# Kernel tuning notes

Measured on AMD Instinct MI355X. Metric: run time of the kernel, lower is better.

Reference implementation:

```python
import jax, jax.numpy as jnp
import numpy as np

# SLAYER SRM-alpha neuron params (nmnist.yaml defaults)
THETA = 10.0      # spike threshold
TAU_SR = 10.0     # PSP (alpha kernel) time constant
TAU_REF = 1.0     # refractory time constant
SCALE_REF = 2.0   # refractory amplitude scale (kernel peak = -2*theta)
TS = 1.0          # simulation step (ms)
K_EPS = 100       # truncated PSP kernel length (alpha kernel ~0 beyond 10*tau)

_t = np.arange(K_EPS, dtype=np.float32) * TS
EPS = jnp.asarray((_t / TAU_SR) * np.exp(1.0 - _t / TAU_SR))  # alpha kernel, peak 1
REF_DECAY = float(np.exp(-TS / TAU_REF))
REF_AMP = SCALE_REF * THETA


def spike_fn(u):
    # hard threshold (forward only)
    return (u >= THETA).astype(u.dtype)


def psp(x):
    """Causal temporal convolution with the SRM alpha kernel. x: [B,C,H,W,T]."""
    B, C, H, W, T = x.shape
    xf = x.reshape(B * C * H * W, 1, T)
    k = EPS[::-1].reshape(1, 1, K_EPS).astype(x.dtype)
    y = jax.lax.conv_general_dilated(xf, k, (1,), [(K_EPS - 1, 0)])
    return y.reshape(B, C, H, W, T)


def spike(a):
    """Threshold with exponential refractory feedback, sequential over time."""
    at = jnp.moveaxis(a, -1, 0)  # [T,B,C,H,W]
    def step(r, a_t):
        u = a_t + r
        s = spike_fn(u)
        r_new = REF_DECAY * (r - REF_AMP * s)
        return r_new, s
    _, s = jax.lax.scan(step, jnp.zeros(at.shape[1:], a.dtype), at)
    return jnp.moveaxis(s, 0, -1)


DN = ('NCHWT', 'OIHWT', 'NCHWT')  # time treated as a size-1-kernel spatial dim

def conv_t(x, w, pad):
    # x: [B,C,H,W,T], w: [O,I,kh,kw] -> spatial conv applied at every time step
    return jax.lax.conv_general_dilated(
        x, w[..., None], (1, 1, 1),
        [(pad, pad), (pad, pad), (0, 0)], dimension_numbers=DN)


def pool_t(x):
    # SLAYER pool: depthwise 2x2 sum-pool with fixed weight 1.1*theta
    C = x.shape[1]
    k = jnp.full((C, 1, 2, 2, 1), 1.1 * THETA, x.dtype)
    return jax.lax.conv_general_dilated(
        x, k, (2, 2, 1), [(0, 0), (0, 0), (0, 0)],
        feature_group_count=C, dimension_numbers=DN)


def setup_inputs() -> dict:
    key = jax.random.key(0)
    ks = jax.random.split(key, 5)
    B, T = 16, 300
    s_in = (jax.random.uniform(ks[0], (B, 2, 34, 34, T)) < 0.05).astype(jnp.float32)
    def w(k, shape, fan):
        return jax.random.normal(k, shape, jnp.float32) * (4.0 / np.sqrt(fan))
    W1 = w(ks[1], (16, 2, 5, 5), 2 * 25)
    W2 = w(ks[2], (32, 16, 3, 3), 16 * 9)
    W3 = w(ks[3], (64, 32, 3, 3), 32 * 9)
    Wf = w(ks[4], (10, 64, 8, 8), 64 * 64)
    return {"s_in": s_in, "W1": W1, "W2": W2, "W3": W3, "Wf": Wf}


def reference(s_in, W1, W2, W3, Wf):
    s1 = spike(psp(conv_t(s_in, W1, 1)))  # [B,16,32,32,T]
    s2 = spike(psp(pool_t(s1)))           # [B,16,16,16,T]
    s3 = spike(psp(conv_t(s2, W2, 1)))    # [B,32,16,16,T]
    s4 = spike(psp(pool_t(s3)))           # [B,32,8,8,T]
    s5 = spike(psp(conv_t(s4, W3, 1)))    # [B,64,8,8,T]
    # dense (8,8,64)->10 is a full-extent conv == contraction over c,h,w
    u = jnp.einsum('bchwt,ochw->bot', s5, Wf)[:, :, None, None, :]
    return spike(psp(u))                  # [B,10,1,1,T]
```

## Files before the change

### kernel.cpp

```cpp
#include <hip/hip_runtime.h>
#include <hip/hip_bf16.h>
#include <stdint.h>
#include <stddef.h>

#define TPAD 320
#define TREAL 300

#define POOL_W   11.000000000000002

typedef double v4d __attribute__((ext_vector_type(4)));

static __device__ __forceinline__ float bf2f(uint16_t b) {
    return __uint_as_float(((uint32_t)b) << 16);
}

struct IIRC { double DD, C1, C2, C3, DR; };
static __device__ __forceinline__ IIRC iirc_make() {
    IIRC c;
    c.DD = exp(-0.1);
    c.C1 = exp(1.0) / 10.0;
    c.C2 = exp(-9.0) / 10.0;
    c.C3 = 10.0 * exp(-9.0);
    c.DR = exp(-1.0);
    return c;
}
struct IIRS { double P, Q, P2, Q2, r; };
static __device__ __forceinline__ void iirs_init(IIRS& s) {
    s.P = 0.0; s.Q = 0.0; s.P2 = 0.0; s.Q2 = 0.0; s.r = 0.0;
}
static __device__ __forceinline__ bool iir_step(const IIRC& c, IIRS& st,
                                                double x, double xd) {
    double Qn  = c.DD * (st.Q + st.P);
    double Pn  = fma(c.DD, st.P, x);
    double Q2n = c.DD * (st.Q2 + st.P2);
    double P2n = fma(c.DD, st.P2, xd);
    double a = c.C1 * Qn - c.C2 * Q2n - c.C3 * P2n;
    double u = a + st.r;
    bool s = (u >= 10.0);
    st.r = c.DR * (st.r - (s ? 20.0 : 0.0));
    st.P = Pn; st.Q = Qn; st.P2 = P2n; st.Q2 = Q2n;
    return s;
}

__global__ void detect_kernel(const uint16_t* __restrict__ w1raw, int* __restrict__ flag)
{
    if (threadIdx.x == 0 && blockIdx.x == 0) {
        int sane = 1;
        for (int i = 0; i < 800; ++i) {
            int e = (w1raw[i] >> 7) & 0xFF;
            if (e >= 131) { sane = 0; break; }
        }
        *flag = sane;
    }
}

static __device__ __forceinline__ double probe_w(int a, int b, int s) {
    uint32_t h = (uint32_t)(a * 73856093) ^ (uint32_t)(b * 19349663)
               ^ (uint32_t)(s * 83492791) ^ 0x9e3779b9u;
    h ^= h >> 13; h *= 0x85ebca6bu; h ^= h >> 16;
    int m = 128 + (int)(h & 127u);
    int e = -12 + (int)((h >> 7) & 7u);
    double v = ldexp((double)m, e);
    return ((h >> 15) & 1u) ? -v : v;
}
static __device__ __forceinline__ double probe_x(int i, int k, int s) {
    return (double)(((i * 5 + k * 3 + s) % 7) < 3 ? 1 : 0);
}
static __device__ __forceinline__ void d_decode(int dvar, int lane, int r,
                                                int& i, int& j) {
    int l15 = lane & 15, l4 = lane >> 4;
    if (dvar == 0)      { i = 4 * l4 + r;  j = l15; }
    else if (dvar == 1) { i = l4 + 4 * r;  j = l15; }
    else                { i = l15;         j = 4 * l4 + r; }
}

__global__ void mfma_probe_kernel(int* __restrict__ mode)
{
    const int lane = (int)threadIdx.x & 63;
    const int l15 = lane & 15;
    const int l4  = lane >> 4;
    int found = 0;
    for (int c = 0; c < 6; ++c) {
        int bvar = c / 3, dvar = c % 3;
        bool ok = true;
        for (int s = 0; s < 4; ++s) {
            double av = probe_x(l15, l4, s);
            double bv = (bvar == 0) ? probe_w(l4, l15, s)
                                    : probe_w(lane & 3, lane >> 2, s);
            v4d cc;
            #pragma unroll
            for (int r = 0; r < 4; ++r) {
                int i, j; d_decode(dvar, lane, r, i, j);
                cc[r] = probe_w(32 + i, j, s + 17);
            }
            v4d d = __builtin_amdgcn_mfma_f64_16x16x4f64(av, bv, cc, 0, 0, 0);
            #pragma unroll
            for (int r = 0; r < 4; ++r) {
                int i, j; d_decode(dvar, lane, r, i, j);
                double e = probe_w(32 + i, j, s + 17);
                #pragma unroll
                for (int k = 0; k < 4; ++k)
                    e = fma(probe_x(i, k, s), probe_w(k, j, s), e);
                ok &= (__double_as_longlong(e) == __double_as_longlong(d[r]));
            }
        }
        unsigned long long bo = __ballot(ok);
        if (bo == ~0ull && found == 0) found = c + 1;
    }
    if (threadIdx.x == 0) *mode = found;
}

__global__ __launch_bounds__(256) void wtrans_kernel(
    const void* __restrict__ w, double* __restrict__ out, int Co, int CKK,
    const int* __restrict__ flag)
{
    int i = blockIdx.x * 256 + threadIdx.x;
    if (i >= Co * CKK) return;
    int co = i / CKK, r = i - co * CKK;
    double v = (*flag) ? (double)bf2f(((const uint16_t*)w)[i])
                       : (double)((const float*)w)[i];
    out[(size_t)(co >> 4) * CKK * 16 + (size_t)r * 16 + (co & 15)] = v;
}

__global__ __launch_bounds__(256) void wtrans_frag_kernel(
    const void* __restrict__ w, double* __restrict__ out,
    int CKK, int KS_TOTAL, int total,
    const int* __restrict__ flag, const int* __restrict__ mode)
{
    int i = blockIdx.x * 256 + threadIdx.x;
    if (i >= total) return;
    int md = *mode;
    int bvar = (md > 0) ? (md - 1) / 3 : 0;
    int lane = i & 63;
    int gks  = (i >> 6) % KS_TOTAL;
    int gy   = (i >> 6) / KS_TOTAL;
    int kl, col;
    if (bvar == 0) { kl = lane >> 4; col = lane & 15; }
    else           { kl = lane & 3;  col = lane >> 2; }
    int tap  = gks * 4 + kl;
    int co   = gy * 16 + col;
    double v = 0.0;
    if (tap < CKK) {
        int src = co * CKK + tap;
        v = (*flag) ? (double)bf2f(((const uint16_t*)w)[src])
                    : (double)((const float*)w)[src];
    }
    out[i] = v;
}

__global__ __launch_bounds__(256) void wcvt_kernel(
    const void* __restrict__ w, float* __restrict__ out, int n, const int* __restrict__ flag)
{
    int i = blockIdx.x * 256 + threadIdx.x;
    if (i >= n) return;
    out[i] = (*flag) ? bf2f(((const uint16_t*)w)[i]) : ((const float*)w)[i];
}

__global__ __launch_bounds__(320) void convert_kernel(
    const void* __restrict__ s_in, uint8_t* __restrict__ u8, const int* __restrict__ flag)
{
    int row = blockIdx.x;
    int t = threadIdx.x;
    uint8_t v = 0;
    if (t < TREAL) {
        float x = (*flag) ? bf2f(((const uint16_t*)s_in)[(size_t)row * TREAL + t])
                          : ((const float*)s_in)[(size_t)row * TREAL + t];
        v = (x >= 0.5f) ? 1 : 0;
    }
    u8[(size_t)row * TPAD + t] = v;
}

template<int Ci, int CIB, int K, int Hi>
__global__ __launch_bounds__(320, 3) void conv_z_kernel(
    const uint8_t* __restrict__ sprev,
    const double* __restrict__ Wt,
    double* __restrict__ z,
    int Co_total, const int* __restrict__ mode)
{
    if (*mode != 0) return;
    constexpr int P = 1;
    constexpr int Wi = Hi;
    constexpr int Ho = Hi + 2 * P - K + 1;
    constexpr int Wo = Ho;
    constexpr int KK = K * K;
    constexpr int CKK = Ci * KK;
    constexpr int CW = K + 1;
    constexpr int NROW = CIB * K * CW;
    constexpr int NPASS = Ci / CIB;
    constexpr int WTILE = CIB * KK * 16;
    static_assert(Ci % CIB == 0, "pass split");
    static_assert(Wo % 2 == 0, "pair split");
    static_assert(NROW * 320 + WTILE * 8 <= 60 * 1024, "LDS over limit");

    __shared__ uint32_t stage[NROW * 80];
    __shared__ double wtile[WTILE];

    const int t   = threadIdx.x;
    const int h   = (int)blockIdx.x / (Wo / 2);
    const int w   = ((int)blockIdx.x % (Wo / 2)) * 2;
    const int gy  = (int)blockIdx.y;
    const int co0 = gy * 16;
    const int b   = (int)blockIdx.z;

    double acc0[16], acc1[16];
    #pragma unroll
    for (int c = 0; c < 16; ++c) { acc0[c] = 0.0; acc1[c] = 0.0; }

    const size_t in_b = (size_t)b * Ci * Hi * Wi * TPAD;
    const double* wg = Wt + (size_t)gy * CKK * 16;

    for (int p = 0; p < NPASS; ++p) {
        const int ci0 = p * CIB;
        __syncthreads();
        for (int idx = t; idx < NROW * 20; idx += 320) {
            int r  = idx / 20, dw = idx - (idx / 20) * 20;
            int cl = r / (K * CW);
            int rem = r - cl * (K * CW);
            int ky = rem / CW, cx = rem - ky * CW;
            int row = h - P + ky;
            int col = w - P + cx;
            uint4 v = make_uint4(0, 0, 0, 0);
            if ((unsigned)row < (unsigned)Hi && (unsigned)col < (unsigned)Wi)
                v = *(const uint4*)(sprev + in_b +
                      (((size_t)(ci0 + cl) * Hi + row) * Wi + col) * TPAD + dw * 16);
            ((uint4*)stage)[(size_t)r * 20 + dw] = v;
        }
        for (int i = t; i < WTILE; i += 320)
            wtile[i] = wg[(size_t)ci0 * KK * 16 + i];
        __syncthreads();

        const uint8_t* sbytes = (const uint8_t*)stage;
        #pragma unroll 2
        for (int cl = 0; cl < CIB; ++cl) {
            #pragma unroll
            for (int ky = 0; ky < K; ++ky) {
                #pragma unroll
                for (int kx = 0; kx < K; ++kx) {
                    const int rbase = ((cl * K + ky) * CW + kx) * 320;
                    double x0 = (double)sbytes[rbase + t];
                    double x1 = (double)sbytes[rbase + 320 + t];
                    const double* wrow = wtile + (cl * KK + ky * K + kx) * 16;
                    #pragma unroll
                    for (int c = 0; c < 16; ++c) {
                        double wv = wrow[c];
                        acc0[c] = fma(wv, x0, acc0[c]);
                        acc1[c] = fma(wv, x1, acc1[c]);
                    }
                }
            }
        }
    }

    #pragma unroll
    for (int c = 0; c < 16; ++c) {
        size_t row0 = (((size_t)b * Co_total + co0 + c) * Ho + h) * Wo + w;
        z[row0 * TPAD + t]          = acc0[c];
        z[(row0 + 1) * TPAD + t]    = acc1[c];
    }
}

template<int Ci, int CIB, int K, int Hi>
__global__ __launch_bounds__(320) void conv_z_mfma_kernel(
    const uint8_t* __restrict__ sprev,
    const double* __restrict__ Wfrag,
    double* __restrict__ z,
    int Co_total, const int* __restrict__ mode)
{
    const int md = *mode;
    if (md == 0) return;
    const int dvar = (md - 1) % 3;
    constexpr int P = 1;
    constexpr int Wi = Hi;
    constexpr int Ho = Hi + 2 * P - K + 1;
    constexpr int Wo = Ho;
    constexpr int KK = K * K;
    constexpr int CW = K + 1;
    constexpr int NROW = CIB * K * CW;
    constexpr int NPASS = Ci / CIB;
    constexpr int TPP = CIB * KK;
    constexpr int KSP = (TPP + 3) / 4;
    constexpr int KS_TOTAL = NPASS * KSP;
    static_assert(Ci % CIB == 0, "pass split");
    static_assert(Wo % 2 == 0, "pair split");
    static_assert(NROW * 320 + KSP * 64 * 8 <= 60 * 1024, "LDS over limit");

    __shared__ uint32_t stage[NROW * 80];
    __shared__ double wtile[KSP * 64];

    const int t    = threadIdx.x;
    const int wave = t >> 6;
    const int lane = t & 63;
    const int l15  = lane & 15;
    const int l4   = lane >> 4;
    const int h    = (int)blockIdx.x / (Wo / 2);
    const int w    = ((int)blockIdx.x % (Wo / 2)) * 2;
    const int gy   = (int)blockIdx.y;
    const int co0  = gy * 16;
    const int b    = (int)blockIdx.z;

    v4d acc[8];
    #pragma unroll
    for (int jj = 0; jj < 8; ++jj) acc[jj] = (v4d)(0.0);

    const size_t in_b = (size_t)b * Ci * Hi * Wi * TPAD;
    const double* wfg = Wfrag + (size_t)gy * KS_TOTAL * 64;

    for (int p = 0; p < NPASS; ++p) {
        const int ci0 = p * CIB;
        __syncthreads();
        for (int idx = t; idx < NROW * 20; idx += 320) {
            int r  = idx / 20, dw = idx - (idx / 20) * 20;
            int cl = r / (K * CW);
            int rem = r - cl * (K * CW);
            int ky = rem / CW, cx = rem - ky * CW;
            int row = h - P + ky;
            int col = w - P + cx;
            uint4 v = make_uint4(0, 0, 0, 0);
            if ((unsigned)row < (unsigned)Hi && (unsigned)col < (unsigned)Wi)
                v = *(const uint4*)(sprev + in_b +
                      (((size_t)(ci0 + cl) * Hi + row) * Wi + col) * TPAD + dw * 16);
            ((uint4*)stage)[(size_t)r * 20 + dw] = v;
        }
        for (int i = t; i < KSP * 64; i += 320)
            wtile[i] = wfg[(size_t)p * KSP * 64 + i];
        __syncthreads();

        const uint8_t* sbytes = (const uint8_t*)stage;
        for (int ks = 0; ks < KSP; ++ks) {
            double bv = wtile[ks * 64 + lane];
            int ltap = ks * 4 + l4;
            int rowoff = 0;
            if ((TPP % 4 == 0) || (ltap < TPP)) {
                int cl  = ltap / KK;
                int rem = ltap - cl * KK;
                int ky  = rem / K;
                int kx  = rem - ky * K;
                rowoff = ((cl * K + ky) * CW + kx) * 320;
            }
            const uint8_t* ab = sbytes + rowoff + l15;
            #pragma unroll
            for (int jj = 0; jj < 8; ++jj) {
                int jb = wave * 8 + jj;
                int tile = jb >> 1, px = jb & 1;
                double av = (double)ab[px * 320 + tile * 16];
                acc[jj] = __builtin_amdgcn_mfma_f64_16x16x4f64(av, bv, acc[jj], 0, 0, 0);
            }
        }
    }

    if (dvar == 0) {
        #pragma unroll
        for (int jj = 0; jj < 8; ++jj) {
            int jb = wave * 8 + jj;
            int tile = jb >> 1, px = jb & 1;
            size_t row = (((size_t)b * Co_total + co0 + l15) * Ho + h) * Wo + w + px;
            *(v4d*)(z + row * TPAD + tile * 16 + l4 * 4) = acc[jj];
        }
    } else if (dvar == 1) {
        #pragma unroll
        for (int jj = 0; jj < 8; ++jj) {
            int jb = wave * 8 + jj;
            int tile = jb >> 1, px = jb & 1;
            size_t row = (((size_t)b * Co_total + co0 + l15) * Ho + h) * Wo + w + px;
            #pragma unroll
            for (int r = 0; r < 4; ++r)
                z[row * TPAD + tile * 16 + l4 + 4 * r] = acc[jj][r];
        }
    } else {
        #pragma unroll
        for (int jj = 0; jj < 8; ++jj) {
            int jb = wave * 8 + jj;
            int tile = jb >> 1, px = jb & 1;
            #pragma unroll
            for (int r = 0; r < 4; ++r) {
                size_t row = (((size_t)b * Co_total + co0 + 4 * l4 + r) * Ho + h) * Wo + w + px;
                z[row * TPAD + tile * 16 + l15] = acc[jj][r];
            }
        }
    }
}

__global__ __launch_bounds__(256) void psp_scan_kernel(
    const double* __restrict__ z, uint8_t* __restrict__ sout, int N)
{
    __shared__ uint32_t bits[64 * 11];
    const int tid = threadIdx.x;
    const int n0 = blockIdx.x * 64;
    const int n = n0 + tid;
    const bool active = (tid < 64) && (n < N);

    if (active) {
        const double* zr = z + (size_t)n * TPAD;
        const IIRC c = iirc_make();
        IIRS st; iirs_init(st);
        uint32_t bw = 0;
        #pragma unroll 5
        for (int t0 = 0; t0 < 100; t0 += 4) {
            double2 xa = *(const double2*)(zr + t0);
            double2 xb = *(const double2*)(zr + t0 + 2);
            if (iir_step(c, st, xa.x, 0.0)) bw |= 1u << (t0 & 31);
            if (iir_step(c, st, xa.y, 0.0)) bw |= 1u << ((t0 + 1) & 31);
            if (iir_step(c, st, xb.x, 0.0)) bw |= 1u << ((t0 + 2) & 31);
            if (iir_step(c, st, xb.y, 0.0)) bw |= 1u << ((t0 + 3) & 31);
            if ((t0 & 31) == 28) { bits[tid * 11 + (t0 >> 5)] = bw; bw = 0; }
        }
        #pragma unroll 5
        for (int t0 = 100; t0 < TREAL; t0 += 4) {
            double2 xa = *(const double2*)(zr + t0);
            double2 xb = *(const double2*)(zr + t0 + 2);
            double2 da = *(const double2*)(zr + t0 - 100);
            double2 db = *(const double2*)(zr + t0 - 98);
            if (iir_step(c, st, xa.x, da.x)) bw |= 1u << (t0 & 31);
            if (iir_step(c, st, xa.y, da.y)) bw |= 1u << ((t0 + 1) & 31);
            if (iir_step(c, st, xb.x, db.x)) bw |= 1u << ((t0 + 2) & 31);
            if (iir_step(c, st, xb.y, db.y)) bw |= 1u << ((t0 + 3) & 31);
            if ((t0 & 31) == 28) { bits[tid * 11 + (t0 >> 5)] = bw; bw = 0; }
        }
        bits[tid * 11 + 9] = bw;
    }
    __syncthreads();

    for (int task = tid; task < 64 * 80; task += 256) {
        int nl = task / 80, w = task - nl * 80;
        int ng = n0 + nl;
        if (ng >= N) continue;
        int tb = w * 4;
        uint32_t word = bits[nl * 11 + (tb >> 5)];
        uint32_t o = 0;
        #pragma unroll
        for (int j = 0; j < 4; ++j)
            if ((word >> ((tb + j) & 31)) & 1u) o |= 1u << (8 * j);
        *(uint32_t*)(sout + (size_t)ng * TPAD + tb) = o;
    }
}

template<int C, int Hi>
__global__ __launch_bounds__(256) void pool_psp_v2_kernel(
    const uint8_t* __restrict__ sprev, uint8_t* __restrict__ sout, int N)
{
    constexpr int Wi = Hi, Ho = Hi / 2, Wo = Wi / 2;
    __shared__ uint32_t cnt[128 * 81];
    __shared__ uint32_t bits[128 * 11];
    const int tid = threadIdx.x;
    const int n0 = blockIdx.x * 128;

    for (int task = tid; task < 128 * 80; task += 256) {
        int nl = task / 80, w = task - nl * 80;
        int n = n0 + nl;
        if (n >= N) continue;
        int wo = n % Wo;  int r1 = n / Wo;
        int ho = r1 % Ho; int r2 = r1 / Ho;
        int cc = r2 % C;  int b  = r2 / C;
        const uint8_t* p0 = sprev +
            ((((size_t)b * C + cc) * Hi + 2 * ho) * Wi + 2 * wo) * TPAD + w * 4;
        uint32_t a0 = *(const uint32_t*)p0;
        uint32_t a1 = *(const uint32_t*)(p0 + TPAD);
        uint32_t a2 = *(const uint32_t*)(p0 + (size_t)Wi * TPAD);
        uint32_t a3 = *(const uint32_t*)(p0 + (size_t)(Wi + 1) * TPAD);
        cnt[nl * 81 + w] = a0 + a1 + a2 + a3;
    }
    __syncthreads();

    if (tid < 128 && n0 + tid < N) {
        const uint8_t* cb = (const uint8_t*)cnt + (size_t)tid * 324;
        const IIRC c = iirc_make();
        IIRS st; iirs_init(st);
        uint32_t bw = 0;
        for (int t = 0; t < 100; ++t) {
            double x = POOL_W * (double)cb[t];
            if (iir_step(c, st, x, 0.0)) bw |= 1u << (t & 31);
            if ((t & 31) == 31) { bits[tid * 11 + (t >> 5)] = bw; bw = 0; }
        }
        for (int t = 100; t < TREAL; ++t) {
            double x  = POOL_W * (double)cb[t];
            double xd = POOL_W * (double)cb[t - 100];
            if (iir_step(c, st, x, xd)) bw |= 1u << (t & 31);
            if ((t & 31) == 31) { bits[tid * 11 + (t >> 5)] = bw; bw = 0; }
        }
        bits[tid * 11 + 9] = bw;
    }
    __syncthreads();

    for (int task = tid; task < 128 * 80; task += 256) {
        int nl = task / 80, w = task - nl * 80;
        int n = n0 + nl;
        if (n >= N) continue;
        int tb = w * 4;
        uint32_t word = bits[nl * 11 + (tb >> 5)];
        uint32_t o = 0;
        #pragma unroll
        for (int j = 0; j < 4; ++j)
            if ((word >> ((tb + j) & 31)) & 1u) o |= 1u << (8 * j);
        *(uint32_t*)(sout + (size_t)n * TPAD + tb) = o;
    }
}

__global__ __launch_bounds__(256) void dense_partial_kernel(
    const uint8_t* __restrict__ s5, const float* __restrict__ Wf,
    double* __restrict__ partial)
{
    const int tc = blockIdx.x, b = blockIdx.y, p = blockIdx.z;
    const int tid = threadIdx.x;
    const int tl = tid & 63, slot = tid >> 6;
    const int t = tc * 64 + tl;
    const int i0 = p * 256 + slot * 64;
    double acc[10];
    #pragma unroll
    for (int o = 0; o < 10; ++o) acc[o] = 0.0;
    const uint8_t* sp = s5 + ((size_t)b * 4096 + i0) * TPAD + t;
    for (int i = 0; i < 64; ++i) {
        float f = (float)sp[(size_t)i * TPAD];
        if (__any(f != 0.f)) {
            #pragma unroll
            for (int o = 0; o < 10; ++o)
                acc[o] = fma((double)Wf[o * 4096 + i0 + i], (double)f, acc[o]);
        }
    }
    __shared__ double red[4][64][10];
    #pragma unroll
    for (int o = 0; o < 10; ++o) red[slot][tl][o] = acc[o];
    __syncthreads();
    if (slot == 0) {
        #pragma unroll
        for (int o = 0; o < 10; ++o) {
            double v = ((red[0][tl][o] + red[1][tl][o]) + red[2][tl][o]) + red[3][tl][o];
            partial[((size_t)p * 160 + (size_t)b * 10 + o) * TPAD + t] = v;
        }
    }
}

__global__ __launch_bounds__(320) void psp_out_final_kernel(
    const double* __restrict__ partial, void* __restrict__ out,
    const int* __restrict__ flag)
{
    __shared__ double xs[TPAD];
    __shared__ uint8_t sb[TREAL];
    const int n = blockIdx.x;
    const int t = threadIdx.x;
    double v = 0.0;
    #pragma unroll
    for (int p = 0; p < 16; ++p)
        v += partial[((size_t)p * 160 + n) * TPAD + t];
    xs[t] = v;
    __syncthreads();
    if (t == 0) {
        const IIRC c = iirc_make();
        IIRS st; iirs_init(st);
        for (int i = 0; i < TREAL; ++i) {
            double xd = (i >= 100) ? xs[i - 100] : 0.0;
            sb[i] = iir_step(c, st, xs[i], xd) ? 1 : 0;
        }
    }
    __syncthreads();
    if (t < TREAL) {
        size_t e = (size_t)n * TREAL + t;
        if (*flag) ((uint16_t*)out)[e] = sb[t] ? 0x3F80 : 0;
        else       ((float*)out)[e]    = sb[t] ? 1.0f : 0.0f;
    }
}

__global__ __launch_bounds__(256) void fill_kernel(float* __restrict__ out, int n, float v)
{
    int i = blockIdx.x * 256 + threadIdx.x;
    if (i < n) out[i] = v;
}

static inline size_t alignup(size_t x) { return (x + 255) & ~(size_t)255; }
static inline int pick_bg(size_t per_b, size_t budget) {
    const int cand[5] = {16, 8, 4, 2, 1};
    for (int k = 0; k < 5; ++k)
        if (per_b * (size_t)cand[k] <= budget) return cand[k];
    return 0;
}

extern "C" void kernel_launch(void* const* d_in, const int* in_sizes, int n_in,
                              void* d_out, int out_size, void* d_ws, size_t ws_size,
                              hipStream_t stream)
{
    if (n_in != 5 || in_sizes[0] != 16 * 2 * 34 * 34 * 300 || in_sizes[1] != 800 ||
        in_sizes[2] != 4608 || in_sizes[3] != 18432 || in_sizes[4] != 40960 ||
        out_size != 16 * 10 * 300) {
        fill_kernel<<<(out_size + 255) / 256, 256, 0, stream>>>((float*)d_out, out_size, 2.0e5f);
        return;
    }

    const size_t flag_sz  = alignup(sizeof(int));
    const size_t mode_sz  = alignup(sizeof(int));
    const size_t w64_sz   = alignup((size_t)(800 + 4608 + 18432) * 8);
    const size_t wfrag_sz = alignup((size_t)(832 + 4608 + 18432) * 8);
    const size_t wf32_sz  = alignup((size_t)40960 * 4);
    const size_t sin8_sz  = alignup((size_t)16 * 2 * 34 * 34 * TPAD);
    const size_t dpart_sz = alignup((size_t)16 * 160 * TPAD * 8);
    const size_t sA_sz    = alignup((size_t)16 * 16384 * TPAD);
    const size_t sB_sz    = alignup((size_t)16 * 4096 * TPAD);
    const size_t base_sz  = flag_sz + mode_sz + w64_sz + wfrag_sz + wf32_sz +
                            sin8_sz + dpart_sz + sA_sz + sB_sz;
    if (base_sz + 256 > ws_size) {
        fill_kernel<<<(out_size + 255) / 256, 256, 0, stream>>>((float*)d_out, out_size, 1.0e5f);
        return;
    }
    const size_t zbud = ws_size - base_sz - 256;

    const size_t zb1 = (size_t)16 * 1024 * TPAD * 8;
    const size_t zb3 = (size_t)32 * 256 * TPAD * 8;
    const size_t zb5 = (size_t)64 * 64 * TPAD * 8;
    const int bg1 = pick_bg(zb1, zbud), bg3 = pick_bg(zb3, zbud), bg5 = pick_bg(zb5, zbud);
    if (bg1 == 0 || bg3 == 0 || bg5 == 0) {
        fill_kernel<<<(out_size + 255) / 256, 256, 0, stream>>>((float*)d_out, out_size, 1.0e5f);
        return;
    }

    char* base = (char*)d_ws;
    int* flag = (int*)base;          base += flag_sz;
    int* mode = (int*)base;          base += mode_sz;
    double* w64 = (double*)base;     base += w64_sz;
    double* wfrag = (double*)base;   base += wfrag_sz;
    float* wf32 = (float*)base;      base += wf32_sz;
    uint8_t* sin8 = (uint8_t*)base;  base += sin8_sz;
    double* dpart = (double*)base;   base += dpart_sz;
    uint8_t* sA = (uint8_t*)base;    base += sA_sz;
    uint8_t* sB = (uint8_t*)base;    base += sB_sz;
    double* z64 = (double*)base;

    detect_kernel<<<1, 64, 0, stream>>>((const uint16_t*)d_in[1], flag);
    mfma_probe_kernel<<<1, 64, 0, stream>>>(mode);

    double* Wt1 = w64;
    double* Wt2 = w64 + 800;
    double* Wt3 = w64 + 800 + 4608;
    wtrans_kernel<<<(800 + 255) / 256, 256, 0, stream>>>(d_in[1], Wt1, 16, 50, flag);
    wtrans_kernel<<<(4608 + 255) / 256, 256, 0, stream>>>(d_in[2], Wt2, 32, 144, flag);
    wtrans_kernel<<<(18432 + 255) / 256, 256, 0, stream>>>(d_in[3], Wt3, 64, 288, flag);

    double* Wf1 = wfrag;
    double* Wf2 = wfrag + 832;
    double* Wf3 = wfrag + 832 + 4608;
    wtrans_frag_kernel<<<(832 + 255) / 256, 256, 0, stream>>>(
        d_in[1], Wf1, 50, 13, 832, flag, mode);
    wtrans_frag_kernel<<<(4608 + 255) / 256, 256, 0, stream>>>(
        d_in[2], Wf2, 144, 36, 4608, flag, mode);
    wtrans_frag_kernel<<<(18432 + 255) / 256, 256, 0, stream>>>(
        d_in[3], Wf3, 288, 72, 18432, flag, mode);

    wcvt_kernel<<<(40960 + 255) / 256, 256, 0, stream>>>(d_in[4], wf32, 40960, flag);
    convert_kernel<<<16 * 2 * 34 * 34, 320, 0, stream>>>(d_in[0], sin8, flag);

    for (int b0 = 0; b0 < 16; b0 += bg1) {
        conv_z_kernel<2, 2, 5, 34><<<dim3(32 * 16, 1, bg1), 320, 0, stream>>>(
            sin8 + (size_t)b0 * 2 * 34 * 34 * TPAD, Wt1, z64, 16, mode);
        conv_z_mfma_kernel<2, 2, 5, 34><<<dim3(32 * 16, 1, bg1), 320, 0, stream>>>(
            sin8 + (size_t)b0 * 2 * 34 * 34 * TPAD, Wf1, z64, 16, mode);
        int N = bg1 * 16384;
        psp_scan_kernel<<<(N + 63) / 64, 256, 0, stream>>>(
            z64, sA + (size_t)b0 * 16384 * TPAD, N);
    }
    pool_psp_v2_kernel<16, 32><<<(16 * 4096 + 127) / 128, 256, 0, stream>>>(
        sA, sB, 16 * 4096);
    for (int b0 = 0; b0 < 16; b0 += bg3) {
        conv_z_kernel<16, 8, 3, 16><<<dim3(16 * 8, 2, bg3), 320, 0, stream>>>(
            sB + (size_t)b0 * 16 * 256 * TPAD, Wt2, z64, 32, mode);
        conv_z_mfma_kernel<16, 8, 3, 16><<<dim3(16 * 8, 2, bg3), 320, 0, stream>>>(
            sB + (size_t)b0 * 16 * 256 * TPAD, Wf2, z64, 32, mode);
        int N = bg3 * 8192;
        psp_scan_kernel<<<(N + 63) / 64, 256, 0, stream>>>(
            z64, sA + (size_t)b0 * 8192 * TPAD, N);
    }
    pool_psp_v2_kernel<32, 16><<<(16 * 2048 + 127) / 128, 256, 0, stream>>>(
        sA, sB, 16 * 2048);
    for (int b0 = 0; b0 < 16; b0 += bg5) {
        conv_z_kernel<32, 8, 3, 8><<<dim3(8 * 4, 4, bg5), 320, 0, stream>>>(
            sB + (size_t)b0 * 32 * 64 * TPAD, Wt3, z64, 64, mode);
        conv_z_mfma_kernel<32, 8, 3, 8><<<dim3(8 * 4, 4, bg5), 320, 0, stream>>>(
            sB + (size_t)b0 * 32 * 64 * TPAD, Wf3, z64, 64, mode);
        int N = bg5 * 4096;
        psp_scan_kernel<<<(N + 63) / 64, 256, 0, stream>>>(
            z64, sA + (size_t)b0 * 4096 * TPAD, N);
    }
    dense_partial_kernel<<<dim3(5, 16, 16), 256, 0, stream>>>(sA, wf32, dpart);
    psp_out_final_kernel<<<160, 320, 0, stream>>>(dpart, d_out, flag);
}
```

Baseline: 1.922 ms.

## Drop LDS staging in MFMA conv; read spikes and weights directly from global

```diff
diff --git a/kernel.cpp b/kernel.cpp
--- a/kernel.cpp
+++ b/kernel.cpp
@@ -259,8 +259,8 @@
     }
 }
 
-template<int Ci, int CIB, int K, int Hi>
-__global__ __launch_bounds__(320) void conv_z_mfma_kernel(
+template<int Ci, int K, int Hi>
+__global__ __launch_bounds__(320, 3) void conv_z_mfma_kernel(
     const uint8_t* __restrict__ sprev,
     const double* __restrict__ Wfrag,
     double* __restrict__ z,
@@ -274,18 +274,9 @@
     constexpr int Ho = Hi + 2 * P - K + 1;
     constexpr int Wo = Ho;
     constexpr int KK = K * K;
-    constexpr int CW = K + 1;
-    constexpr int NROW = CIB * K * CW;
-    constexpr int NPASS = Ci / CIB;
-    constexpr int TPP = CIB * KK;
-    constexpr int KSP = (TPP + 3) / 4;
-    constexpr int KS_TOTAL = NPASS * KSP;
-    static_assert(Ci % CIB == 0, "pass split");
+    constexpr int CKK = Ci * KK;
+    constexpr int KS_TOTAL = (CKK + 3) / 4;
     static_assert(Wo % 2 == 0, "pair split");
-    static_assert(NROW * 320 + KSP * 64 * 8 <= 60 * 1024, "LDS over limit");
-
-    __shared__ uint32_t stage[NROW * 80];
-    __shared__ double wtile[KSP * 64];
 
     const int t    = threadIdx.x;
     const int wave = t >> 6;
@@ -302,49 +293,35 @@
     #pragma unroll
     for (int jj = 0; jj < 8; ++jj) acc[jj] = (v4d)(0.0);
 
-    const size_t in_b = (size_t)b * Ci * Hi * Wi * TPAD;
-    const double* wfg = Wfrag + (size_t)gy * KS_TOTAL * 64;
-
-    for (int p = 0; p < NPASS; ++p) {
-        const int ci0 = p * CIB;
-        __syncthreads();
-        for (int idx = t; idx < NROW * 20; idx += 320) {
-            int r  = idx / 20, dw = idx - (idx / 20) * 20;
-            int cl = r / (K * CW);
-            int rem = r - cl * (K * CW);
-            int ky = rem / CW, cx = rem - ky * CW;
-            int row = h - P + ky;
-            int col = w - P + cx;
-            uint4 v = make_uint4(0, 0, 0, 0);
-            if ((unsigned)row < (unsigned)Hi && (unsigned)col < (unsigned)Wi)
-                v = *(const uint4*)(sprev + in_b +
-                      (((size_t)(ci0 + cl) * Hi + row) * Wi + col) * TPAD + dw * 16);
-            ((uint4*)stage)[(size_t)r * 20 + dw] = v;
-        }
-        for (int i = t; i < KSP * 64; i += 320)
-            wtile[i] = wfg[(size_t)p * KSP * 64 + i];
-        __syncthreads();
-
-        const uint8_t* sbytes = (const uint8_t*)stage;
-        for (int ks = 0; ks < KSP; ++ks) {
-            double bv = wtile[ks * 64 + lane];
-            int ltap = ks * 4 + l4;
-            int rowoff = 0;
-            if ((TPP % 4 == 0) || (ltap < TPP)) {
-                int cl  = ltap / KK;
-                int rem = ltap - cl * KK;
-                int ky  = rem / K;
-                int kx  = rem - ky * K;
-                rowoff = ((cl * K + ky) * CW + kx) * 320;
-            }
-            const uint8_t* ab = sbytes + rowoff + l15;
-            #pragma unroll
-            for (int jj = 0; jj < 8; ++jj) {
-                int jb = wave * 8 + jj;
-                int tile = jb >> 1, px = jb & 1;
-                double av = (double)ab[px * 320 + tile * 16];
-                acc[jj] = __builtin_amdgcn_mfma_f64_16x16x4f64(av, bv, acc[jj], 0, 0, 0);
-            }
+    const uint8_t* sp_b = sprev + (size_t)b * Ci * Hi * Wi * TPAD;
+    const double* wf = Wfrag + (size_t)gy * KS_TOTAL * 64 + lane;
+
+    for (int gks = 0; gks < KS_TOTAL; ++gks) {
+        double bv = wf[(size_t)gks * 64];
+        int ltap = gks * 4 + l4;
+        int ci  = ltap / KK;
+        int rem = ltap - ci * KK;
+        int ky  = rem / K;
+        int kx  = rem - ky * K;
+        int row = h - P + ky;
+        int col = w - P + kx;
+        bool tv = (CKK % 4 == 0) || (ltap < CKK);
+        bool vr = tv && ((unsigned)row < (unsigned)Hi);
+        bool v0 = vr && ((unsigned)col < (unsigned)Wi);
+        bool v1 = vr && ((unsigned)(col + 1) < (unsigned)Wi);
+        int cic  = tv ? ci : 0;
+        int rowc = vr ? row : 0;
+        int c0   = v0 ? col : 0;
+        int c1   = v1 ? (col + 1) : 0;
+        const uint8_t* p0 = sp_b + (((size_t)cic * Hi + rowc) * Wi + c0) * TPAD + l15;
+        const uint8_t* p1 = sp_b + (((size_t)cic * Hi + rowc) * Wi + c1) * TPAD + l15;
+        #pragma unroll
+        for (int q = 0; q < 4; ++q) {
+            int tile = wave * 4 + q;
+            double a0 = v0 ? (double)p0[tile * 16] : 0.0;
+            acc[2 * q] = __builtin_amdgcn_mfma_f64_16x16x4f64(a0, bv, acc[2 * q], 0, 0, 0);
+            double a1 = v1 ? (double)p1[tile * 16] : 0.0;
+            acc[2 * q + 1] = __builtin_amdgcn_mfma_f64_16x16x4f64(a1, bv, acc[2 * q + 1], 0, 0, 0);
         }
     }
 
@@ -648,7 +625,7 @@
     for (int b0 = 0; b0 < 16; b0 += bg1) {
         conv_z_kernel<2, 2, 5, 34><<<dim3(32 * 16, 1, bg1), 320, 0, stream>>>(
             sin8 + (size_t)b0 * 2 * 34 * 34 * TPAD, Wt1, z64, 16, mode);
-        conv_z_mfma_kernel<2, 2, 5, 34><<<dim3(32 * 16, 1, bg1), 320, 0, stream>>>(
+        conv_z_mfma_kernel<2, 5, 34><<<dim3(32 * 16, 1, bg1), 320, 0, stream>>>(
             sin8 + (size_t)b0 * 2 * 34 * 34 * TPAD, Wf1, z64, 16, mode);
         int N = bg1 * 16384;
         psp_scan_kernel<<<(N + 63) / 64, 256, 0, stream>>>(
@@ -659,7 +636,7 @@
     for (int b0 = 0; b0 < 16; b0 += bg3) {
         conv_z_kernel<16, 8, 3, 16><<<dim3(16 * 8, 2, bg3), 320, 0, stream>>>(
             sB + (size_t)b0 * 16 * 256 * TPAD, Wt2, z64, 32, mode);
-        conv_z_mfma_kernel<16, 8, 3, 16><<<dim3(16 * 8, 2, bg3), 320, 0, stream>>>(
+        conv_z_mfma_kernel<16, 3, 16><<<dim3(16 * 8, 2, bg3), 320, 0, stream>>>(
             sB + (size_t)b0 * 16 * 256 * TPAD, Wf2, z64, 32, mode);
         int N = bg3 * 8192;
         psp_scan_kernel<<<(N + 63) / 64, 256, 0, stream>>>(
@@ -670,7 +647,7 @@
     for (int b0 = 0; b0 < 16; b0 += bg5) {
         conv_z_kernel<32, 8, 3, 8><<<dim3(8 * 4, 4, bg5), 320, 0, stream>>>(
             sB + (size_t)b0 * 32 * 64 * TPAD, Wt3, z64, 64, mode);
-        conv_z_mfma_kernel<32, 8, 3, 8><<<dim3(8 * 4, 4, bg5), 320, 0, stream>>>(
+        conv_z_mfma_kernel<32, 3, 8><<<dim3(8 * 4, 4, bg5), 320, 0, stream>>>(
             sB + (size_t)b0 * 32 * 64 * TPAD, Wf3, z64, 64, mode);
         int N = bg5 * 4096;
         psp_scan_kernel<<<(N + 63) / 64, 256, 0, stream>>>(
```

Measured after the change: 2.522 ms. +31.2%, slower.
